# Performance work log

Measured on AMD Instinct MI355X. Metric: run time of the kernel, lower is better.

## Reference

```python
import jax, jax.numpy as jnp
import numpy as np

USER_NUM = 60000
ITEM_NUM = 40000
NODE_NUM = USER_NUM + ITEM_NUM
EMBED_DIM = 64
N_LAYER = 3
NNZ = 1600000
BATCH = 4096
NEG_SLOPE = 0.2


def setup_inputs() -> dict:
    key = jax.random.key(0)
    ks = jax.random.split(key, 8)
    emb = jax.random.normal(ks[0], (NODE_NUM, EMBED_DIM), dtype=jnp.float32) * 0.1
    W1 = jax.random.normal(ks[1], (N_LAYER, EMBED_DIM, EMBED_DIM), dtype=jnp.float32) * 0.1
    W2 = jax.random.normal(ks[2], (N_LAYER, EMBED_DIM, EMBED_DIM), dtype=jnp.float32) * 0.1
    vals = jax.random.uniform(ks[3], (NNZ,), dtype=jnp.float32) * 0.01  # normalized Laplacian weights
    row_idx = jax.random.randint(ks[4], (NNZ,), 0, NODE_NUM, dtype=jnp.int32)
    col_idx = jax.random.randint(ks[5], (NNZ,), 0, NODE_NUM, dtype=jnp.int32)
    user_idx = jax.random.randint(ks[6], (BATCH,), 0, USER_NUM, dtype=jnp.int32)
    item_idx = jax.random.randint(ks[7], (BATCH,), 0, ITEM_NUM, dtype=jnp.int32)
    return {"emb": emb, "W1": W1, "W2": W2, "vals": vals,
            "row_idx": row_idx, "col_idx": col_idx,
            "user_idx": user_idx, "item_idx": item_idx}


def _spmm(vals, row_idx, col_idx, E):
    # L @ E with L in COO form: gather source rows, scale, scatter-add to dest rows
    msgs = vals[:, None] * E[col_idx]                       # [nnz, D]
    return jax.ops.segment_sum(msgs, row_idx, num_segments=NODE_NUM)


def reference(emb, W1, W2, vals, row_idx, col_idx, user_idx, item_idx):
    E_prev = emb
    E_list = [emb]
    for layer in range(N_LAYER):
        side_E = _spmm(vals, row_idx, col_idx, E_prev)      # [N, D]
        sum_E = side_E + E_prev
        bi_E = E_prev * side_E
        E_next = jax.nn.leaky_relu(sum_E @ W1[layer] + bi_E @ W2[layer],
                                   negative_slope=NEG_SLOPE)
        # dropout=0.0 / eval mode -> no-op
        E_prev = E_next
        E_list.append(E_next)
    E_all = jnp.concatenate(E_list, axis=1)                 # [N, D*(L+1)]
    E_user = E_all[:USER_NUM]
    E_item = E_all[USER_NUM:]
    return (E_user[user_idx], E_item[item_idx])
```

## Files before the change

kernel.cpp:

```cpp
#include <hip/hip_runtime.h>
#include <hip/hip_bf16.h>

#define USER_NUM 60000
#define ITEM_NUM 40000
#define NODE_NUM 100000
#define DIM 64
#define NNZ_N 1600000
#define BATCH 4096
#define NEG 0.2f
#define NBKT 98
#define PA_EPT 16
#define PA_EPB (256 * PA_EPT)
#define PA_GRID ((NNZ_N + PA_EPB - 1) / PA_EPB)
#define VAL_DEC 3.0517578125e-07f
#define NTILE 6250

typedef unsigned long long u64;
typedef unsigned int u32;
typedef __attribute__((ext_vector_type(8))) short bf16x8;
typedef __attribute__((ext_vector_type(4))) float f32x4;
typedef __attribute__((ext_vector_type(2))) float f32x2;

__device__ __forceinline__ float bf2f(unsigned short u) {
    return __uint_as_float(((u32)u) << 16);
}
__device__ __forceinline__ unsigned short f2bf(float f) {
    u32 x = __float_as_uint(f);
    u32 r = (x + 0x7FFFu + ((x >> 16) & 1u)) >> 16;
    return (unsigned short)r;
}
template <bool WORD>
__device__ __forceinline__ int cvt2fp8(u32 u, int old) {
    float lo = __uint_as_float(u << 16);
    float hi = __uint_as_float(u & 0xffff0000u);
    return __builtin_amdgcn_cvt_pk_fp8_f32(lo, hi, old, WORD);
}

__global__ void k_bcount(const int* __restrict__ row, int* __restrict__ bkt_cnt, int n) {
    __shared__ int h[NBKT];
    int t = threadIdx.x;
    if (t < NBKT) h[t] = 0;
    __syncthreads();
    int base = blockIdx.x * PA_EPB;
#pragma unroll
    for (int j = 0; j < PA_EPT; j++) {
        int idx = base + j * 256 + t;
        if (idx < n) atomicAdd(&h[row[idx] >> 10], 1);
    }
    __syncthreads();
    if (t < NBKT && h[t]) atomicAdd(&bkt_cnt[t], h[t]);
}

__global__ void k_bscan(const int* __restrict__ bkt_cnt, int* __restrict__ bkt_base,
                        int* __restrict__ bcur) {
    __shared__ int sh[128];
    int t = threadIdx.x;
    int v = (t < NBKT) ? bkt_cnt[t] : 0;
    sh[t] = v;
    __syncthreads();
    for (int d = 1; d < 128; d <<= 1) {
        int x = (t >= d) ? sh[t - d] : 0;
        __syncthreads();
        sh[t] += x;
        __syncthreads();
    }
    int excl = sh[t] - v;
    if (t < NBKT) { bkt_base[t] = excl; bcur[t] = excl; }
    if (t == 0) bkt_base[NBKT] = NNZ_N;
}

__launch_bounds__(256)
__global__ void k_passA(const int* __restrict__ row, const int* __restrict__ col,
                        const float* __restrict__ vals, int* __restrict__ bcur,
                        u64* __restrict__ tpk, int n) {
    __shared__ int cur[NBKT];
    __shared__ int gb[NBKT];
    int t = threadIdx.x;
    if (t < NBKT) cur[t] = 0;
    __syncthreads();
    int base = blockIdx.x * PA_EPB;
    u64 pk[PA_EPT];
    int rk[PA_EPT], bk[PA_EPT];
#pragma unroll
    for (int j = 0; j < PA_EPT; j++) {
        int idx = base + j * 256 + t;
        if (idx < n) {
            int r = row[idx];
            int c = col[idx];
            int bits = (int)rintf(vals[idx] * 3276800.0f);
            if (bits > 32767) bits = 32767;
            pk[j] = ((u64)(u32)r << 32) | ((u32)c << 15) | (u32)bits;
            bk[j] = r >> 10;
            rk[j] = atomicAdd(&cur[bk[j]], 1);
        } else bk[j] = -1;
    }
    __syncthreads();
    if (t < NBKT) {
        int cnt = cur[t];
        gb[t] = cnt ? atomicAdd(&bcur[t], cnt) : 0;
    }
    __syncthreads();
#pragma unroll
    for (int j = 0; j < PA_EPT; j++) {
        if (bk[j] >= 0) tpk[gb[bk[j]] + rk[j]] = pk[j];
    }
}

__launch_bounds__(1024)
__global__ void k_passB(const u64* __restrict__ tpk, const int* __restrict__ bkt_base,
                        int* __restrict__ ptr, u32* __restrict__ ecv,
                        int* __restrict__ dhist) {
    __shared__ int sh[1024];
    __shared__ int h2[64];
    int b = blockIdx.x, t = threadIdx.x;
    int start = bkt_base[b], end = bkt_base[b + 1];
    sh[t] = 0;
    if (t < 64) h2[t] = 0;
    __syncthreads();
    for (int i = start + t; i < end; i += 1024)
        atomicAdd(&sh[(int)(tpk[i] >> 32) & 1023], 1);
    __syncthreads();
    int cnt = sh[t];
    int rowg = (b << 10) + t;
    if (rowg < NODE_NUM) atomicAdd(&h2[cnt > 63 ? 63 : cnt], 1);
    for (int d = 1; d < 1024; d <<= 1) {
        int x = (t >= d) ? sh[t - d] : 0;
        __syncthreads();
        sh[t] += x;
        __syncthreads();
    }
    int excl = sh[t] - cnt;
    if (rowg < NODE_NUM) ptr[rowg] = start + excl;
    if (b == NBKT - 1 && t == 0) ptr[NODE_NUM] = NNZ_N;
    __syncthreads();
    sh[t] = excl;
    __syncthreads();
    for (int i = start + t; i < end; i += 1024) {
        u64 e = tpk[i];
        int r = (int)(e >> 32);
        int pos = start + atomicAdd(&sh[r & 1023], 1);
        ecv[pos] = (u32)e;
    }
    __syncthreads();
    if (t < 64 && h2[t]) atomicAdd(&dhist[t], h2[t]);
}

__global__ void k_dscan(const int* __restrict__ dhist, int* __restrict__ dcur) {
    __shared__ int sh[64];
    int t = threadIdx.x;
    int v = dhist[t];
    sh[t] = v;
    __syncthreads();
    for (int d = 1; d < 64; d <<= 1) {
        int x = (t >= d) ? sh[t - d] : 0;
        __syncthreads();
        sh[t] += x;
        __syncthreads();
    }
    dcur[t] = sh[t] - v;
}

__launch_bounds__(1024)
__global__ void k_dscatter(const int* __restrict__ ptr, int* __restrict__ dcur,
                           int* __restrict__ rord, int n) {
    __shared__ int h[64];
    __shared__ int gb[64];
    int t = threadIdx.x;
    if (t < 64) h[t] = 0;
    __syncthreads();
    int i = blockIdx.x * 1024 + t;
    int d = -1, rk = 0;
    if (i < n) {
        d = ptr[i + 1] - ptr[i];
        if (d > 63) d = 63;
        rk = atomicAdd(&h[d], 1);
    }
    __syncthreads();
    if (t < 64) {
        int cnt = h[t];
        gb[t] = cnt ? atomicAdd(&dcur[t], cnt) : 0;
    }
    __syncthreads();
    if (i < n) rord[gb[d] + rk] = i;
}

__global__ void k_cvt4(const float4* __restrict__ src, ushort4* __restrict__ dstB,
                       u32* __restrict__ dstF, int n4) {
    int i = blockIdx.x * 256 + threadIdx.x;
    if (i < n4) {
        float4 f = src[i];
        dstB[i] = make_ushort4(f2bf(f.x), f2bf(f.y), f2bf(f.z), f2bf(f.w));
        int w = __builtin_amdgcn_cvt_pk_fp8_f32(f.x, f.y, 0, false);
        w = __builtin_amdgcn_cvt_pk_fp8_f32(f.z, f.w, w, true);
        dstF[i] = (u32)w;
    }
}

__launch_bounds__(256)
__global__ void k_spmm(const int* __restrict__ ptrS, const int* __restrict__ rord,
                       const u32* __restrict__ ecv, const unsigned char* __restrict__ Ef,
                       unsigned short* __restrict__ S) {
    int wave = (blockIdx.x * 256 + threadIdx.x) >> 6;
    int lane = threadIdx.x & 63;
    int L = lane & 7;
    int rslot = wave * 8 + (lane >> 3);
    int myrow = rord[rslot];
    int s = ptrS[myrow];
    int e = ptrS[myrow + 1];
    int dm = e - s;
    dm = max(dm, __shfl_xor(dm, 8));
    dm = max(dm, __shfl_xor(dm, 16));
    dm = max(dm, __shfl_xor(dm, 32));
    float acc[8];
#pragma unroll
    for (int q = 0; q < 8; q++) acc[q] = 0.f;
    int srcbase = lane & 56;
    for (int off = 0; off < dm; off += 8) {
        int idx = s + off + L;
        u32 u = (idx < e) ? ecv[idx] : 0u;
#pragma unroll
        for (int j = 0; j < 8; j++) {
            u32 uu = __shfl(u, srcbase | j);
            float fv = (float)(uu & 0x7fffu);
            uint2 gw = *(const uint2*)&Ef[(size_t)(uu >> 15) * 64 + L * 8];
            f32x2 g01 = __builtin_amdgcn_cvt_pk_f32_fp8(gw.x, false);
            f32x2 g23 = __builtin_amdgcn_cvt_pk_f32_fp8(gw.x, true);
            f32x2 g45 = __builtin_amdgcn_cvt_pk_f32_fp8(gw.y, false);
            f32x2 g67 = __builtin_amdgcn_cvt_pk_f32_fp8(gw.y, true);
            acc[0] = fmaf(fv, g01.x, acc[0]);
            acc[1] = fmaf(fv, g01.y, acc[1]);
            acc[2] = fmaf(fv, g23.x, acc[2]);
            acc[3] = fmaf(fv, g23.y, acc[3]);
            acc[4] = fmaf(fv, g45.x, acc[4]);
            acc[5] = fmaf(fv, g45.y, acc[5]);
            acc[6] = fmaf(fv, g67.x, acc[6]);
            acc[7] = fmaf(fv, g67.y, acc[7]);
        }
    }
    u32 o[4];
#pragma unroll
    for (int q = 0; q < 4; q++) {
        float x0 = acc[2 * q] * VAL_DEC;
        float x1 = acc[2 * q + 1] * VAL_DEC;
        o[q] = (u32)f2bf(x0) | ((u32)f2bf(x1) << 16);
    }
    *(uint4*)&S[(size_t)myrow * 64 + L * 8] = make_uint4(o[0], o[1], o[2], o[3]);
}

__launch_bounds__(256)
__global__ void k_dmm(const unsigned short* __restrict__ Ein,
                      const unsigned short* __restrict__ S,
                      const float* __restrict__ W1l, const float* __restrict__ W2l,
                      unsigned short* __restrict__ Eout, unsigned char* __restrict__ Eout8) {
    __shared__ unsigned short cbuf[4][16 * 68];
    int t = threadIdx.x;
    int w = t >> 6;
    int lane = t & 63;
    int r16 = lane & 15;
    int g = lane >> 4;

    bf16x8 bw[2][2][4];
#pragma unroll
    for (int mat = 0; mat < 2; mat++) {
        const float* W = mat ? W2l : W1l;
#pragma unroll
        for (int kc = 0; kc < 2; kc++) {
#pragma unroll
            for (int cb = 0; cb < 4; cb++) {
                int col = cb * 16 + r16;
                int k0 = kc * 32 + g * 8;
                bf16x8 f;
#pragma unroll
                for (int j = 0; j < 8; j++)
                    f[j] = (short)f2bf(W[(k0 + j) * 64 + col]);
                bw[mat][kc][cb] = f;
            }
        }
    }

    for (int tile = blockIdx.x * 4 + w; tile < NTILE; tile += gridDim.x * 4) {
        int row0 = tile * 16;
        const unsigned short* ep = &Ein[(size_t)(row0 + r16) * 64 + g * 8];
        const unsigned short* sp = &S[(size_t)(row0 + r16) * 64 + g * 8];
        f32x4 ac0 = {0.f, 0.f, 0.f, 0.f};
        f32x4 ac1 = {0.f, 0.f, 0.f, 0.f};
        f32x4 ac2 = {0.f, 0.f, 0.f, 0.f};
        f32x4 ac3 = {0.f, 0.f, 0.f, 0.f};
#pragma unroll
        for (int kc = 0; kc < 2; kc++) {
            bf16x8 ev = *(const bf16x8*)(ep + kc * 32);
            bf16x8 sv = *(const bf16x8*)(sp + kc * 32);
            bf16x8 su, bi;
#pragma unroll
            for (int j = 0; j < 8; j++) {
                float e = bf2f((unsigned short)ev[j]);
                float s = bf2f((unsigned short)sv[j]);
                su[j] = (short)f2bf(e + s);
                bi[j] = (short)f2bf(e * s);
            }
            ac0 = __builtin_amdgcn_mfma_f32_16x16x32_bf16(su, bw[0][kc][0], ac0, 0, 0, 0);
            ac0 = __builtin_amdgcn_mfma_f32_16x16x32_bf16(bi, bw[1][kc][0], ac0, 0, 0, 0);
            ac1 = __builtin_amdgcn_mfma_f32_16x16x32_bf16(su, bw[0][kc][1], ac1, 0, 0, 0);
            ac1 = __builtin_amdgcn_mfma_f32_16x16x32_bf16(bi, bw[1][kc][1], ac1, 0, 0, 0);
            ac2 = __builtin_amdgcn_mfma_f32_16x16x32_bf16(su, bw[0][kc][2], ac2, 0, 0, 0);
            ac2 = __builtin_amdgcn_mfma_f32_16x16x32_bf16(bi, bw[1][kc][2], ac2, 0, 0, 0);
            ac3 = __builtin_amdgcn_mfma_f32_16x16x32_bf16(su, bw[0][kc][3], ac3, 0, 0, 0);
            ac3 = __builtin_amdgcn_mfma_f32_16x16x32_bf16(bi, bw[1][kc][3], ac3, 0, 0, 0);
        }
#pragma unroll
        for (int reg = 0; reg < 4; reg++) {
            int crow = g * 4 + reg;
            float x0 = ac0[reg]; x0 = x0 > 0.f ? x0 : NEG * x0;
            float x1 = ac1[reg]; x1 = x1 > 0.f ? x1 : NEG * x1;
            float x2 = ac2[reg]; x2 = x2 > 0.f ? x2 : NEG * x2;
            float x3 = ac3[reg]; x3 = x3 > 0.f ? x3 : NEG * x3;
            cbuf[w][crow * 68 + 0 * 16 + r16] = f2bf(x0);
            cbuf[w][crow * 68 + 1 * 16 + r16] = f2bf(x1);
            cbuf[w][crow * 68 + 2 * 16 + r16] = f2bf(x2);
            cbuf[w][crow * 68 + 3 * 16 + r16] = f2bf(x3);
        }
        int rrow = lane >> 2;
        int q = lane & 3;
        const uint4* lp = (const uint4*)&cbuf[w][rrow * 68 + q * 16];
        uint4 v0 = lp[0];
        uint4 v1 = lp[1];
        uint4* gp = (uint4*)&Eout[(size_t)(row0 + rrow) * 64 + q * 16];
        gp[0] = v0;
        gp[1] = v1;
        int w0 = cvt2fp8<false>(v0.x, 0); w0 = cvt2fp8<true>(v0.y, w0);
        int w1 = cvt2fp8<false>(v0.z, 0); w1 = cvt2fp8<true>(v0.w, w1);
        int w2 = cvt2fp8<false>(v1.x, 0); w2 = cvt2fp8<true>(v1.y, w2);
        int w3 = cvt2fp8<false>(v1.z, 0); w3 = cvt2fp8<true>(v1.w, w3);
        *(uint4*)&Eout8[(size_t)(row0 + rrow) * 64 + q * 16] =
            make_uint4((u32)w0, (u32)w1, (u32)w2, (u32)w3);
    }
}

__global__ void k_gather0(const float* __restrict__ E, float* __restrict__ out,
                          const int* __restrict__ uidx, const int* __restrict__ iidx) {
    int g = blockIdx.x * 256 + threadIdx.x;
    int b = g >> 6, d = g & 63;
    if (b >= 2 * BATCH) return;
    int node;
    size_t obase;
    if (b < BATCH) { node = uidx[b]; obase = (size_t)b * 256; }
    else { int bb = b - BATCH; node = USER_NUM + iidx[bb]; obase = (size_t)BATCH * 256 + (size_t)bb * 256; }
    out[obase + d] = E[(size_t)node * 64 + d];
}

__global__ void k_gatherb(const unsigned short* __restrict__ E, float* __restrict__ out,
                          const int* __restrict__ uidx, const int* __restrict__ iidx,
                          int layer) {
    int g = blockIdx.x * 256 + threadIdx.x;
    int b = g >> 6, d = g & 63;
    if (b >= 2 * BATCH) return;
    int node;
    size_t obase;
    if (b < BATCH) { node = uidx[b]; obase = (size_t)b * 256; }
    else { int bb = b - BATCH; node = USER_NUM + iidx[bb]; obase = (size_t)BATCH * 256 + (size_t)bb * 256; }
    out[obase + layer * 64 + d] = bf2f(E[(size_t)node * 64 + d]);
}

extern "C" void kernel_launch(void* const* d_in, const int* in_sizes, int n_in,
                              void* d_out, int out_size, void* d_ws, size_t ws_size,
                              hipStream_t stream) {
    const float* emb  = (const float*)d_in[0];
    const float* W1   = (const float*)d_in[1];
    const float* W2   = (const float*)d_in[2];
    const float* vals = (const float*)d_in[3];
    const int*   row  = (const int*)d_in[4];
    const int*   col  = (const int*)d_in[5];
    const int*   uidx = (const int*)d_in[6];
    const int*   iidx = (const int*)d_in[7];
    float* out = (float*)d_out;

    char* p = (char*)d_ws;
    auto alloc = [&](size_t bytes) -> void* {
        void* q = (void*)p;
        p += (bytes + 255) & ~(size_t)255;
        return q;
    };
    int*            ptr      = (int*)alloc((size_t)(NODE_NUM + 1) * 4);
    int*            bkt_cnt  = (int*)alloc(NBKT * 4);
    int*            bkt_base = (int*)alloc((NBKT + 1) * 4);
    int*            bcur     = (int*)alloc(NBKT * 4);
    int*            dhist    = (int*)alloc(64 * 4);
    int*            dcur     = (int*)alloc(64 * 4);
    int*            rord     = (int*)alloc((size_t)NODE_NUM * 4);
    u32*            ecv      = (u32*)alloc((size_t)NNZ_N * 4);
    u64*            tpk      = (u64*)alloc((size_t)NNZ_N * 8);
    unsigned short* Sb       = (unsigned short*)alloc((size_t)NODE_NUM * DIM * 2);
    unsigned short* Ebf0     = (unsigned short*)alloc((size_t)NODE_NUM * DIM * 2);
    unsigned short* Eba      = (unsigned short*)alloc((size_t)NODE_NUM * DIM * 2);
    unsigned short* Ebb      = (unsigned short*)alloc((size_t)NODE_NUM * DIM * 2);
    unsigned char*  Ef0      = (unsigned char*)alloc((size_t)NODE_NUM * DIM);
    unsigned char*  Efa      = (unsigned char*)alloc((size_t)NODE_NUM * DIM);
    unsigned char*  Efb      = (unsigned char*)alloc((size_t)NODE_NUM * DIM);

    hipMemsetAsync(bkt_cnt, 0, NBKT * 4, stream);
    hipMemsetAsync(dhist, 0, 64 * 4, stream);
    k_bcount<<<PA_GRID, 256, 0, stream>>>(row, bkt_cnt, NNZ_N);
    k_bscan<<<1, 128, 0, stream>>>(bkt_cnt, bkt_base, bcur);
    k_passA<<<PA_GRID, 256, 0, stream>>>(row, col, vals, bcur, tpk, NNZ_N);
    k_passB<<<NBKT, 1024, 0, stream>>>(tpk, bkt_base, ptr, ecv, dhist);

    k_dscan<<<1, 64, 0, stream>>>(dhist, dcur);
    k_dscatter<<<NBKT, 1024, 0, stream>>>(ptr, dcur, rord, NODE_NUM);

    k_cvt4<<<(NODE_NUM * DIM / 4 + 255) / 256, 256, 0, stream>>>(
        (const float4*)emb, (ushort4*)Ebf0, (u32*)Ef0, NODE_NUM * DIM / 4);

    k_gather0<<<2048, 256, 0, stream>>>(emb, out, uidx, iidx);

    const int SPMM_GRID = NODE_NUM / 32;
    const int DMM_GRID = 391;
    k_spmm<<<SPMM_GRID, 256, 0, stream>>>(ptr, rord, ecv, Ef0, Sb);
    k_dmm<<<DMM_GRID, 256, 0, stream>>>(Ebf0, Sb, W1, W2, Eba, Efa);
    k_gatherb<<<2048, 256, 0, stream>>>(Eba, out, uidx, iidx, 1);

    k_spmm<<<SPMM_GRID, 256, 0, stream>>>(ptr, rord, ecv, Efa, Sb);
    k_dmm<<<DMM_GRID, 256, 0, stream>>>(Eba, Sb, W1 + 4096, W2 + 4096, Ebb, Efb);
    k_gatherb<<<2048, 256, 0, stream>>>(Ebb, out, uidx, iidx, 2);

    k_spmm<<<SPMM_GRID, 256, 0, stream>>>(ptr, rord, ecv, Efb, Sb);
    k_dmm<<<DMM_GRID, 256, 0, stream>>>(Ebb, Sb, W1 + 8192, W2 + 8192, Eba, Efa);
    k_gatherb<<<2048, 256, 0, stream>>>(Eba, out, uidx, iidx, 3);
}
```

Baseline: 205.7 us.

## Fold scans into consumers, localize degree sort, merge gathers, skip final fp8

Drops the separate bucket-scan, degree-scan and degree-scatter kernels. Each passA and passB block now recomputes the bucket prefix sum redundantly, and passB sorts rows by degree within its own bucket instead of globally. The four per-layer gathers become one gather at the end, which needs a third bf16 buffer aliased onto the tpk workspace, and the last layer skips its unused fp8 output. The aim is to cut launch count and serial tiny kernels, at the cost of a coarser degree ordering that may hurt spmm load balance.

```diff
diff --git a/kernel.cpp b/kernel.cpp
--- a/kernel.cpp
+++ b/kernel.cpp
@@ -51,32 +51,26 @@
     if (t < NBKT && h[t]) atomicAdd(&bkt_cnt[t], h[t]);
 }
 
-__global__ void k_bscan(const int* __restrict__ bkt_cnt, int* __restrict__ bkt_base,
-                        int* __restrict__ bcur) {
-    __shared__ int sh[128];
-    int t = threadIdx.x;
-    int v = (t < NBKT) ? bkt_cnt[t] : 0;
-    sh[t] = v;
-    __syncthreads();
-    for (int d = 1; d < 128; d <<= 1) {
-        int x = (t >= d) ? sh[t - d] : 0;
-        __syncthreads();
-        sh[t] += x;
-        __syncthreads();
-    }
-    int excl = sh[t] - v;
-    if (t < NBKT) { bkt_base[t] = excl; bcur[t] = excl; }
-    if (t == 0) bkt_base[NBKT] = NNZ_N;
-}
-
 __launch_bounds__(256)
 __global__ void k_passA(const int* __restrict__ row, const int* __restrict__ col,
-                        const float* __restrict__ vals, int* __restrict__ bcur,
-                        u64* __restrict__ tpk, int n) {
+                        const float* __restrict__ vals, const int* __restrict__ bkt_cnt,
+                        int* __restrict__ bcur0, u64* __restrict__ tpk, int n) {
+    __shared__ int sb[128];
+    __shared__ int gbase[NBKT];
     __shared__ int cur[NBKT];
     __shared__ int gb[NBKT];
     int t = threadIdx.x;
+    if (t < 128) sb[t] = (t < NBKT) ? bkt_cnt[t] : 0;
     if (t < NBKT) cur[t] = 0;
+    __syncthreads();
+    for (int d = 1; d < 128; d <<= 1) {
+        int x = 0;
+        if (t < 128 && t >= d) x = sb[t - d];
+        __syncthreads();
+        if (t < 128) sb[t] += x;
+        __syncthreads();
+    }
+    if (t < NBKT) gbase[t] = sb[t] - bkt_cnt[t];
     __syncthreads();
     int base = blockIdx.x * PA_EPB;
     u64 pk[PA_EPT];
@@ -97,7 +91,7 @@
     __syncthreads();
     if (t < NBKT) {
         int cnt = cur[t];
-        gb[t] = cnt ? atomicAdd(&bcur[t], cnt) : 0;
+        gb[t] = gbase[t] + (cnt ? atomicAdd(&bcur0[t], cnt) : 0);
     }
     __syncthreads();
 #pragma unroll
@@ -107,22 +101,35 @@
 }
 
 __launch_bounds__(1024)
-__global__ void k_passB(const u64* __restrict__ tpk, const int* __restrict__ bkt_base,
+__global__ void k_passB(const u64* __restrict__ tpk, const int* __restrict__ bkt_cnt,
                         int* __restrict__ ptr, u32* __restrict__ ecv,
-                        int* __restrict__ dhist) {
+                        int* __restrict__ rord) {
     __shared__ int sh[1024];
+    __shared__ int sb[128];
     __shared__ int h2[64];
+    __shared__ int h2c[64];
     int b = blockIdx.x, t = threadIdx.x;
-    int start = bkt_base[b], end = bkt_base[b + 1];
+    if (t < 128) sb[t] = (t < NBKT) ? bkt_cnt[t] : 0;
+    if (t < 64) { h2[t] = 0; h2c[t] = 0; }
     sh[t] = 0;
-    if (t < 64) h2[t] = 0;
-    __syncthreads();
+    __syncthreads();
+    for (int d = 1; d < 128; d <<= 1) {
+        int x = 0;
+        if (t < 128 && t >= d) x = sb[t - d];
+        __syncthreads();
+        if (t < 128) sb[t] += x;
+        __syncthreads();
+    }
+    int start = sb[b] - bkt_cnt[b];
+    int end = sb[b];
     for (int i = start + t; i < end; i += 1024)
         atomicAdd(&sh[(int)(tpk[i] >> 32) & 1023], 1);
     __syncthreads();
     int cnt = sh[t];
     int rowg = (b << 10) + t;
-    if (rowg < NODE_NUM) atomicAdd(&h2[cnt > 63 ? 63 : cnt], 1);
+    bool valid = (rowg < NODE_NUM);
+    int bin = cnt > 63 ? 63 : cnt;
+    if (valid) atomicAdd(&h2[bin], 1);
     for (int d = 1; d < 1024; d <<= 1) {
         int x = (t >= d) ? sh[t - d] : 0;
         __syncthreads();
@@ -130,7 +137,7 @@
         __syncthreads();
     }
     int excl = sh[t] - cnt;
-    if (rowg < NODE_NUM) ptr[rowg] = start + excl;
+    if (valid) ptr[rowg] = start + excl;
     if (b == NBKT - 1 && t == 0) ptr[NODE_NUM] = NNZ_N;
     __syncthreads();
     sh[t] = excl;
@@ -142,46 +149,20 @@
         ecv[pos] = (u32)e;
     }
     __syncthreads();
-    if (t < 64 && h2[t]) atomicAdd(&dhist[t], h2[t]);
-}
-
-__global__ void k_dscan(const int* __restrict__ dhist, int* __restrict__ dcur) {
-    __shared__ int sh[64];
-    int t = threadIdx.x;
-    int v = dhist[t];
-    sh[t] = v;
+    if (t < 64) sb[t] = h2[t];
     __syncthreads();
     for (int d = 1; d < 64; d <<= 1) {
-        int x = (t >= d) ? sh[t - d] : 0;
-        __syncthreads();
-        sh[t] += x;
-        __syncthreads();
-    }
-    dcur[t] = sh[t] - v;
-}
-
-__launch_bounds__(1024)
-__global__ void k_dscatter(const int* __restrict__ ptr, int* __restrict__ dcur,
-                           int* __restrict__ rord, int n) {
-    __shared__ int h[64];
-    __shared__ int gb[64];
-    int t = threadIdx.x;
-    if (t < 64) h[t] = 0;
-    __syncthreads();
-    int i = blockIdx.x * 1024 + t;
-    int d = -1, rk = 0;
-    if (i < n) {
-        d = ptr[i + 1] - ptr[i];
-        if (d > 63) d = 63;
-        rk = atomicAdd(&h[d], 1);
-    }
-    __syncthreads();
-    if (t < 64) {
-        int cnt = h[t];
-        gb[t] = cnt ? atomicAdd(&dcur[t], cnt) : 0;
-    }
-    __syncthreads();
-    if (i < n) rord[gb[d] + rk] = i;
+        int x = 0;
+        if (t < 64 && t >= d) x = sb[t - d];
+        __syncthreads();
+        if (t < 64) sb[t] += x;
+        __syncthreads();
+    }
+    if (valid) {
+        int h2base = sb[bin] - h2[bin];
+        int rank = atomicAdd(&h2c[bin], 1);
+        rord[(b << 10) + h2base + rank] = rowg;
+    }
 }
 
 __global__ void k_cvt4(const float4* __restrict__ src, ushort4* __restrict__ dstB,
@@ -327,17 +308,23 @@
         uint4* gp = (uint4*)&Eout[(size_t)(row0 + rrow) * 64 + q * 16];
         gp[0] = v0;
         gp[1] = v1;
-        int w0 = cvt2fp8<false>(v0.x, 0); w0 = cvt2fp8<true>(v0.y, w0);
-        int w1 = cvt2fp8<false>(v0.z, 0); w1 = cvt2fp8<true>(v0.w, w1);
-        int w2 = cvt2fp8<false>(v1.x, 0); w2 = cvt2fp8<true>(v1.y, w2);
-        int w3 = cvt2fp8<false>(v1.z, 0); w3 = cvt2fp8<true>(v1.w, w3);
-        *(uint4*)&Eout8[(size_t)(row0 + rrow) * 64 + q * 16] =
-            make_uint4((u32)w0, (u32)w1, (u32)w2, (u32)w3);
-    }
-}
-
-__global__ void k_gather0(const float* __restrict__ E, float* __restrict__ out,
-                          const int* __restrict__ uidx, const int* __restrict__ iidx) {
+        if (Eout8 != nullptr) {
+            int w0 = cvt2fp8<false>(v0.x, 0); w0 = cvt2fp8<true>(v0.y, w0);
+            int w1 = cvt2fp8<false>(v0.z, 0); w1 = cvt2fp8<true>(v0.w, w1);
+            int w2 = cvt2fp8<false>(v1.x, 0); w2 = cvt2fp8<true>(v1.y, w2);
+            int w3 = cvt2fp8<false>(v1.z, 0); w3 = cvt2fp8<true>(v1.w, w3);
+            *(uint4*)&Eout8[(size_t)(row0 + rrow) * 64 + q * 16] =
+                make_uint4((u32)w0, (u32)w1, (u32)w2, (u32)w3);
+        }
+    }
+}
+
+__global__ void k_gatherAll(const float* __restrict__ emb,
+                            const unsigned short* __restrict__ E1,
+                            const unsigned short* __restrict__ E2,
+                            const unsigned short* __restrict__ E3,
+                            float* __restrict__ out,
+                            const int* __restrict__ uidx, const int* __restrict__ iidx) {
     int g = blockIdx.x * 256 + threadIdx.x;
     int b = g >> 6, d = g & 63;
     if (b >= 2 * BATCH) return;
@@ -345,20 +332,11 @@
     size_t obase;
     if (b < BATCH) { node = uidx[b]; obase = (size_t)b * 256; }
     else { int bb = b - BATCH; node = USER_NUM + iidx[bb]; obase = (size_t)BATCH * 256 + (size_t)bb * 256; }
-    out[obase + d] = E[(size_t)node * 64 + d];
-}
-
-__global__ void k_gatherb(const unsigned short* __restrict__ E, float* __restrict__ out,
-                          const int* __restrict__ uidx, const int* __restrict__ iidx,
-                          int layer) {
-    int g = blockIdx.x * 256 + threadIdx.x;
-    int b = g >> 6, d = g & 63;
-    if (b >= 2 * BATCH) return;
-    int node;
-    size_t obase;
-    if (b < BATCH) { node = uidx[b]; obase = (size_t)b * 256; }
-    else { int bb = b - BATCH; node = USER_NUM + iidx[bb]; obase = (size_t)BATCH * 256 + (size_t)bb * 256; }
-    out[obase + layer * 64 + d] = bf2f(E[(size_t)node * 64 + d]);
+    size_t nb = (size_t)node * 64 + d;
+    out[obase + d]       = emb[nb];
+    out[obase + 64 + d]  = bf2f(E1[nb]);
+    out[obase + 128 + d] = bf2f(E2[nb]);
+    out[obase + 192 + d] = bf2f(E3[nb]);
 }
 
 extern "C" void kernel_launch(void* const* d_in, const int* in_sizes, int n_in,
@@ -381,11 +359,7 @@
         return q;
     };
     int*            ptr      = (int*)alloc((size_t)(NODE_NUM + 1) * 4);
-    int*            bkt_cnt  = (int*)alloc(NBKT * 4);
-    int*            bkt_base = (int*)alloc((NBKT + 1) * 4);
-    int*            bcur     = (int*)alloc(NBKT * 4);
-    int*            dhist    = (int*)alloc(64 * 4);
-    int*            dcur     = (int*)alloc(64 * 4);
+    int*            bcnt_cur = (int*)alloc(256 * 4);
     int*            rord     = (int*)alloc((size_t)NODE_NUM * 4);
     u32*            ecv      = (u32*)alloc((size_t)NNZ_N * 4);
     u64*            tpk      = (u64*)alloc((size_t)NNZ_N * 8);
@@ -396,33 +370,28 @@
     unsigned char*  Ef0      = (unsigned char*)alloc((size_t)NODE_NUM * DIM);
     unsigned char*  Efa      = (unsigned char*)alloc((size_t)NODE_NUM * DIM);
     unsigned char*  Efb      = (unsigned char*)alloc((size_t)NODE_NUM * DIM);
-
-    hipMemsetAsync(bkt_cnt, 0, NBKT * 4, stream);
-    hipMemsetAsync(dhist, 0, 64 * 4, stream);
+    int* bkt_cnt = bcnt_cur;
+    int* bcur0   = bcnt_cur + 128;
+    unsigned short* Ebc = (unsigned short*)tpk;
+
+    hipMemsetAsync(bcnt_cur, 0, 256 * 4, stream);
     k_bcount<<<PA_GRID, 256, 0, stream>>>(row, bkt_cnt, NNZ_N);
-    k_bscan<<<1, 128, 0, stream>>>(bkt_cnt, bkt_base, bcur);
-    k_passA<<<PA_GRID, 256, 0, stream>>>(row, col, vals, bcur, tpk, NNZ_N);
-    k_passB<<<NBKT, 1024, 0, stream>>>(tpk, bkt_base, ptr, ecv, dhist);
-
-    k_dscan<<<1, 64, 0, stream>>>(dhist, dcur);
-    k_dscatter<<<NBKT, 1024, 0, stream>>>(ptr, dcur, rord, NODE_NUM);
+    k_passA<<<PA_GRID, 256, 0, stream>>>(row, col, vals, bkt_cnt, bcur0, tpk, NNZ_N);
+    k_passB<<<NBKT, 1024, 0, stream>>>(tpk, bkt_cnt, ptr, ecv, rord);
 
     k_cvt4<<<(NODE_NUM * DIM / 4 + 255) / 256, 256, 0, stream>>>(
         (const float4*)emb, (ushort4*)Ebf0, (u32*)Ef0, NODE_NUM * DIM / 4);
-
-    k_gather0<<<2048, 256, 0, stream>>>(emb, out, uidx, iidx);
 
     const int SPMM_GRID = NODE_NUM / 32;
     const int DMM_GRID = 391;
     k_spmm<<<SPMM_GRID, 256, 0, stream>>>(ptr, rord, ecv, Ef0, Sb);
     k_dmm<<<DMM_GRID, 256, 0, stream>>>(Ebf0, Sb, W1, W2, Eba, Efa);
-    k_gatherb<<<2048, 256, 0, stream>>>(Eba, out, uidx, iidx, 1);
 
     k_spmm<<<SPMM_GRID, 256, 0, stream>>>(ptr, rord, ecv, Efa, Sb);
-    k_dmm<<<DMM_GRID, 256, 0, stream>>>(Eba, Sb, W1 + 4096, W2 + 4096, Ebb, Efb);
-    k_gatherb<<<2048, 256, 0, stream>>>(Ebb, out, uidx, iidx, 2);
+    k_dmm<<<DMM_GRID, 256, 0, stream>>>(Eba, Sb, W1 + 4096, W2 + 4096, Ebc, Efb);
 
     k_spmm<<<SPMM_GRID, 256, 0, stream>>>(ptr, rord, ecv, Efb, Sb);
-    k_dmm<<<DMM_GRID, 256, 0, stream>>>(Ebb, Sb, W1 + 8192, W2 + 8192, Eba, Efa);
-    k_gatherb<<<2048, 256, 0, stream>>>(Eba, out, uidx, iidx, 3);
-}
+    k_dmm<<<DMM_GRID, 256, 0, stream>>>(Ebc, Sb, W1 + 8192, W2 + 8192, Ebb, (unsigned char*)nullptr);
+
+    k_gatherAll<<<2048, 256, 0, stream>>>(emb, Eba, Ebc, Ebb, out, uidx, iidx);
+}
```

New measurement: 199.6 us. 1.03x faster.
